# Kernel tuning notes

Hardware: AMD Instinct MI355X
Metric: run time of the kernel (lower is better)

Reference implementation:

```python
import jax, jax.numpy as jnp
import numpy as np
from jax import lax

K = 3        # kernel_size
PAD = 1      # padding
STRIDE = 1   # stride


def conv2d(x, w, stride, pad):
    return lax.conv_general_dilated(
        x, w, (stride, stride), [(pad, pad), (pad, pad)],
        dimension_numbers=('NCHW', 'OIHW', 'NCHW'))


def setup_inputs() -> dict:
    key = jax.random.key(0)
    ks = jax.random.split(key, 8)
    B, Ci, Cc, H, W = 8, 64, 64, 128, 128
    K2 = K * K
    return {
        'x_img': jax.random.normal(ks[0], (B, Ci, H, W), jnp.float32),
        'x_cont': jax.random.normal(ks[1], (B, Cc, H, W), jnp.float32),
        'w_fuse': jax.random.normal(ks[2], (Ci, Ci + Cc, 1, 1), jnp.float32) * 0.05,
        'w_off': jax.random.normal(ks[3], (2 * K2, Ci, K, K), jnp.float32) * 0.01,
        'b_off': jax.random.normal(ks[4], (2 * K2,), jnp.float32) * 0.1,
        'w_mod': jax.random.normal(ks[5], (K2, Ci, K, K), jnp.float32) * 0.01,
        'b_mod': jax.random.normal(ks[6], (K2,), jnp.float32) * 0.1,
        'w_reg': jax.random.normal(ks[7], (Ci, Ci, K, K), jnp.float32) * 0.05,
    }


def _bilinear_sample(img, py, px):
    # Zero padding outside the image (per-corner validity, matches torchvision).
    C, Hin, Win = img.shape
    flat = img.reshape(C, -1)
    y0 = jnp.floor(py)
    x0 = jnp.floor(px)

    def gather(yy, xx):
        valid = (yy >= 0) & (yy <= Hin - 1) & (xx >= 0) & (xx <= Win - 1)
        yc = jnp.clip(yy, 0, Hin - 1).astype(jnp.int32)
        xc = jnp.clip(xx, 0, Win - 1).astype(jnp.int32)
        return flat[:, yc * Win + xc] * valid[None].astype(img.dtype)

    wy1 = py - y0; wy0 = 1.0 - wy1
    wx1 = px - x0; wx0 = 1.0 - wx1
    return (gather(y0, x0) * (wy0 * wx0)[None]
            + gather(y0, x0 + 1.0) * (wy0 * wx1)[None]
            + gather(y0 + 1.0, x0) * (wy1 * wx0)[None]
            + gather(y0 + 1.0, x0 + 1.0) * (wy1 * wx1)[None])


def reference(x_img, x_cont, w_fuse, w_off, b_off, w_mod, b_mod, w_reg):
    # 1x1 fuse of image features with control factor
    x = conv2d(jnp.concatenate([x_img, x_cont], axis=1), w_fuse, 1, 0)
    # offset / modulator branches
    off = conv2d(x, w_off, STRIDE, PAD) + b_off[None, :, None, None]
    mod = 2.0 * jax.nn.sigmoid(conv2d(x, w_mod, STRIDE, PAD) + b_mod[None, :, None, None])
    B, C, Hin, Win = x.shape
    K2 = K * K
    Hout, Wout = off.shape[2], off.shape[3]
    # torchvision layout: channel 2k = dy, 2k+1 = dx for kernel pos k = i*K + j
    off = off.reshape(B, K2, 2, Hout, Wout)
    dy, dx = off[:, :, 0], off[:, :, 1]
    ky = (jnp.arange(K2) // K).astype(x.dtype)
    kx = (jnp.arange(K2) % K).astype(x.dtype)
    base_y = (jnp.arange(Hout) * STRIDE - PAD).astype(x.dtype)
    base_x = (jnp.arange(Wout) * STRIDE - PAD).astype(x.dtype)
    py = dy + base_y[None, None, :, None] + ky[None, :, None, None]  # [B,K2,H,W]
    px = dx + base_x[None, None, None, :] + kx[None, :, None, None]
    sampled = jax.vmap(_bilinear_sample)(x, py, px)          # [B,C,K2,H,W]
    sampled = sampled * mod[:, None]                          # modulation
    out = jnp.einsum('oik,bikhw->bohw', w_reg.reshape(C, C, K2), sampled)
    return out
```

## Files before the change

### kernel.cpp

```cpp
#include <hip/hip_runtime.h>
#include <math.h>

#define B_   8
#define C_   64
#define H_   128
#define W_   128
#define HW_  16384
#define K2_  9

typedef float f32x4 __attribute__((ext_vector_type(4)));
typedef short bf16x8 __attribute__((ext_vector_type(8)));
typedef unsigned short u16x4 __attribute__((ext_vector_type(4)));

#define WS_WFA  0
#define WS_WRP  8192
#define WS_WRP2 26624
#define WS_XT   45056
#define WS_OM   8433664

static __device__ __forceinline__ unsigned short f2bf(float x) {
    unsigned int u = __float_as_uint(x);
    unsigned int r = (u + 0x7fffu + ((u >> 16) & 1u)) >> 16;
    return (unsigned short)r;
}
static __device__ __forceinline__ float bf2f(unsigned short u) {
    return __uint_as_float(((unsigned int)u) << 16);
}

__global__ __launch_bounds__(256) void k_pack(const float* __restrict__ wf,
                                              const float* __restrict__ wreg,
                                              const float* __restrict__ wOff,
                                              const float* __restrict__ wMod,
                                              unsigned short* __restrict__ wfA,
                                              unsigned short* __restrict__ wrP,
                                              unsigned short* __restrict__ wrP2) {
    int idx = blockIdx.x * 256 + threadIdx.x;
    if (idx < 1024) {
        int lane = idx & 63, mt = (idx >> 6) & 3, kc = idx >> 8;
        int m = mt * 16 + (lane & 15);
        int kb = kc * 32 + (lane >> 4) * 8;
#pragma unroll
        for (int j = 0; j < 8; ++j)
            wfA[idx * 8 + j] = f2bf(wf[m * 128 + kb + j]);
    }
    if (idx < 4608) {
        int lane = idx & 63, mt = (idx >> 6) & 3, kc = (idx >> 8) & 1, tap = idx >> 9;
        int o = mt * 16 + (lane & 15);
        int ibase = kc * 32 + (lane >> 4) * 8;
#pragma unroll
        for (int j = 0; j < 8; ++j)
            wrP[idx * 8 + j] = f2bf(wreg[(o * 64 + ibase + j) * 9 + tap]);
    }
    if (idx < 2304) {
        int lane = idx & 63, mt = (idx >> 6) & 1, kc = idx >> 7;
        int m = mt * 16 + (lane & 15);
        int gkb = kc * 32 + (lane >> 4) * 8;
#pragma unroll
        for (int j = 0; j < 8; ++j) {
            int gk = gkb + j, tap = gk >> 6, ci = gk & 63;
            float v = 0.f;
            if (m < 18)      v = wOff[(m * 64 + ci) * 9 + tap];
            else if (m < 27) v = wMod[((m - 18) * 64 + ci) * 9 + tap];
            wrP2[idx * 8 + j] = f2bf(v);
        }
    }
}

__global__ __launch_bounds__(256) void k_fuse(const float* __restrict__ xi,
                                              const float* __restrict__ xc,
                                              const unsigned short* __restrict__ wfA,
                                              unsigned short* __restrict__ xtb) {
    const int t = threadIdx.x;
    const int lane = t & 63;
    const int wv = t >> 6;
    const int b = blockIdx.x & 7;
    const int yh = blockIdx.x >> 3;
    const int y = yh >> 1;
    const int h = yh & 1;

    const int n15 = lane & 15;
    const int q4 = lane >> 4;
    const int px = h * 64 + wv * 16 + n15;
    const size_t poff = (size_t)y * W_ + px;

    f32x4 acc[4];
#pragma unroll
    for (int mt = 0; mt < 4; ++mt) acc[mt] = (f32x4){0.f, 0.f, 0.f, 0.f};

#pragma unroll
    for (int kc = 0; kc < 4; ++kc) {
        const float* src = (kc < 2)
            ? (xi + ((size_t)(b * 64 + kc * 32 + q4 * 8)) * HW_ + poff)
            : (xc + ((size_t)(b * 64 + (kc - 2) * 32 + q4 * 8)) * HW_ + poff);
        unsigned short us[8];
#pragma unroll
        for (int j = 0; j < 8; ++j) us[j] = f2bf(src[(size_t)j * HW_]);
        const bf16x8 bf = *(const bf16x8*)us;
#pragma unroll
        for (int mt = 0; mt < 4; ++mt) {
            const bf16x8 a = *(const bf16x8*)(wfA + ((size_t)(kc * 4 + mt) * 64 + lane) * 8);
            acc[mt] = __builtin_amdgcn_mfma_f32_16x16x32_bf16(a, bf, acc[mt], 0, 0, 0);
        }
    }

#pragma unroll
    for (int mt = 0; mt < 4; ++mt) {
        u16x4 o4;
        o4.x = f2bf(acc[mt][0]); o4.y = f2bf(acc[mt][1]);
        o4.z = f2bf(acc[mt][2]); o4.w = f2bf(acc[mt][3]);
        *(u16x4*)&xtb[((size_t)b * HW_ + poff) * 64 + mt * 16 + q4 * 4] = o4;
    }
}

__global__ __launch_bounds__(256) void k_offmod(const unsigned short* __restrict__ xtb,
                                                const unsigned short* __restrict__ wrP2,
                                                const float* __restrict__ bOff,
                                                const float* __restrict__ bMod,
                                                float* __restrict__ om) {
    __shared__ unsigned short sB[3 * 66 * 72];
    const int t = threadIdx.x;
    const int lane = t & 63;
    const int wv = t >> 6;
    const int b = blockIdx.x & 7;
    const int yh = blockIdx.x >> 3;
    const int y = yh >> 1;
    const int h = yh & 1;

    for (int idx = t; idx < 3 * 66 * 8; idx += 256) {
        const int c8 = idx & 7;
        const int pp = (idx >> 3) % 66;
        const int row = (idx >> 3) / 66;
        const int gx = h * 64 + pp - 1;
        const int gy = y + row - 1;
        bf16x8 v = {0, 0, 0, 0, 0, 0, 0, 0};
        if (gx >= 0 && gx < W_ && gy >= 0 && gy < H_)
            v = *(const bf16x8*)&xtb[(((size_t)(b * H_ + gy)) * W_ + gx) * 64 + c8 * 8];
        *(bf16x8*)&sB[(row * 66 + pp) * 72 + c8 * 8] = v;
    }
    __syncthreads();

    const int n15 = lane & 15;
    const int q4 = lane >> 4;

    f32x4 acc[2];
    acc[0] = (f32x4){0.f, 0.f, 0.f, 0.f};
    acc[1] = (f32x4){0.f, 0.f, 0.f, 0.f};

#pragma unroll
    for (int kc = 0; kc < 18; ++kc) {
        const int gkb = kc * 32 + q4 * 8;
        const int tap = gkb >> 6;
        const int ci = gkb & 63;
        const int row = tap / 3, kx = tap % 3;
        const bf16x8 bf = *(const bf16x8*)&sB[(row * 66 + (wv * 16 + n15 + kx)) * 72 + ci];
        const bf16x8 a0 = *(const bf16x8*)(wrP2 + (((size_t)(kc * 2 + 0) * 64 + lane) * 8));
        const bf16x8 a1 = *(const bf16x8*)(wrP2 + (((size_t)(kc * 2 + 1) * 64 + lane) * 8));
        acc[0] = __builtin_amdgcn_mfma_f32_16x16x32_bf16(a0, bf, acc[0], 0, 0, 0);
        acc[1] = __builtin_amdgcn_mfma_f32_16x16x32_bf16(a1, bf, acc[1], 0, 0, 0);
    }

    const int px = h * 64 + wv * 16 + n15;
    const size_t rec = ((size_t)(b * H_ + y)) * 28 * 128;
#pragma unroll
    for (int mt = 0; mt < 2; ++mt)
#pragma unroll
        for (int r = 0; r < 4; ++r) {
            const int o = mt * 16 + q4 * 4 + r;
            if (o < 18) {
                const int c = (o >> 1) + ((o & 1) ? 9 : 0);
                om[rec + c * 128 + px] = acc[mt][r] + bOff[o];
            } else if (o < 27) {
                const float z = acc[mt][r] + bMod[o - 18];
                om[rec + (18 + (o - 18)) * 128 + px] = 2.f / (1.f + expf(-z));
            }
        }
}

__global__ __launch_bounds__(256) void k_deform(const unsigned short* __restrict__ xtb,
                                                const float* __restrict__ om,
                                                const unsigned short* __restrict__ wrP,
                                                float* __restrict__ out) {
    __shared__ unsigned short sS2[8 * 520];
    __shared__ unsigned int sRec[4 * 16 * 8];
    const int t = threadIdx.x;
    const int lane = t & 63;
    const int wv = t >> 6;
    const int b = blockIdx.x & 7;
    const int yh = blockIdx.x >> 3;
    const int y = yh >> 1;
    const int h = yh & 1;

    const char* xbB = (const char*)(xtb + (size_t)b * HW_ * 64);
    const float* omr = om + ((size_t)(b * H_ + y)) * 28 * 128;

    const int n15 = lane & 15;
    const int q4 = lane >> 4;
    const int pA = lane >> 2;
    const int corner = lane & 3;
    const int cy = corner >> 1, cx = corner & 1;

    f32x4 acc[4];
#pragma unroll
    for (int mt = 0; mt < 4; ++mt) acc[mt] = (f32x4){0.f, 0.f, 0.f, 0.f};

    for (int k = 0; k < 9; ++k) {
        const int ky = k / 3 - 1, kx = k % 3 - 1;

        {
            const int px = h * 64 + wv * 16 + pA;
            const float dy = omr[k * 128 + px];
            const float dxv = omr[(9 + k) * 128 + px];
            const float m = omr[(18 + k) * 128 + px];
            const float py  = (float)(y + ky) + dy;
            const float pxe = (float)(px + kx) + dxv;
            const float y0f = floorf(py), x0f = floorf(pxe);
            const int y0i = (int)y0f, x0i = (int)x0f;
            const float wy1 = py - y0f, wx1 = pxe - x0f;
            const int yy = y0i + cy;
            const int xx = x0i + cx;
            const bool ok = (yy >= 0) && (yy < H_) && (xx >= 0) && (xx < W_);
            const int yc = min(max(yy, 0), H_ - 1);
            const int xc = min(max(xx, 0), W_ - 1);
            const float w = (cy ? wy1 : 1.f - wy1) * (cx ? wx1 : 1.f - wx1) * m;
            uint2 rec;
            rec.x = (unsigned int)((yc * W_ + xc) * 128);
            rec.y = __float_as_uint(ok ? w : 0.f);
            *(uint2*)&sRec[((wv * 16 + pA) * 4 + corner) * 2] = rec;
        }

#pragma unroll 4
        for (int p = 0; p < 16; ++p) {
            const uint4 r0 = *(const uint4*)&sRec[(wv * 16 + p) * 8];
            const uint4 r1 = *(const uint4*)&sRec[(wv * 16 + p) * 8 + 4];
            const float g0 = bf2f(*(const unsigned short*)(xbB + (r0.x + lane * 2)));
            const float g1 = bf2f(*(const unsigned short*)(xbB + (r0.z + lane * 2)));
            const float g2 = bf2f(*(const unsigned short*)(xbB + (r1.x + lane * 2)));
            const float g3 = bf2f(*(const unsigned short*)(xbB + (r1.z + lane * 2)));
            const float v = g0 * __uint_as_float(r0.y) + g1 * __uint_as_float(r0.w)
                          + g2 * __uint_as_float(r1.y) + g3 * __uint_as_float(r1.w);
            sS2[(lane >> 3) * 520 + (wv * 16 + p) * 8 + (lane & 7)] = f2bf(v);
        }

#pragma unroll
        for (int kc = 0; kc < 2; ++kc) {
            const bf16x8 bf = *(const bf16x8*)&sS2[(kc * 4 + q4) * 520 + (wv * 16 + n15) * 8];
#pragma unroll
            for (int mt = 0; mt < 4; ++mt) {
                const bf16x8 a = *(const bf16x8*)(wrP +
                    ((((size_t)((k * 2 + kc) * 4 + mt)) * 64 + lane) * 8));
                acc[mt] = __builtin_amdgcn_mfma_f32_16x16x32_bf16(a, bf, acc[mt], 0, 0, 0);
            }
        }
    }

    const int px = h * 64 + wv * 16 + n15;
#pragma unroll
    for (int mt = 0; mt < 4; ++mt)
#pragma unroll
        for (int r = 0; r < 4; ++r) {
            const int o = mt * 16 + q4 * 4 + r;
            out[(((size_t)(b * 64 + o)) * H_ + y) * W_ + px] = acc[mt][r];
        }
}

extern "C" void kernel_launch(void* const* d_in, const int* in_sizes, int n_in,
                              void* d_out, int out_size, void* d_ws, size_t ws_size,
                              hipStream_t stream) {
    const float* x_img  = (const float*)d_in[0];
    const float* x_cont = (const float*)d_in[1];
    const float* w_fuse = (const float*)d_in[2];
    const float* w_off  = (const float*)d_in[3];
    const float* b_off  = (const float*)d_in[4];
    const float* w_mod  = (const float*)d_in[5];
    const float* b_mod  = (const float*)d_in[6];
    const float* w_reg  = (const float*)d_in[7];
    float* out = (float*)d_out;

    float* ws  = (float*)d_ws;
    unsigned short* wfA  = (unsigned short*)(ws + WS_WFA);
    unsigned short* wrP  = (unsigned short*)(ws + WS_WRP);
    unsigned short* wrP2 = (unsigned short*)(ws + WS_WRP2);
    unsigned short* xtb  = (unsigned short*)(ws + WS_XT);
    float* om  = ws + WS_OM;

    k_pack<<<18, 256, 0, stream>>>(w_fuse, w_reg, w_off, w_mod, wfA, wrP, wrP2);
    k_fuse<<<B_ * H_ * 2, 256, 0, stream>>>(x_img, x_cont, wfA, xtb);
    k_offmod<<<B_ * H_ * 2, 256, 0, stream>>>(xtb, wrP2, b_off, b_mod, om);
    k_deform<<<B_ * H_ * 2, 256, 0, stream>>>(xtb, om, wrP, out);
}
```

Before: 226.9 us.

## Fold weight packing into fuse kernel and use readlane for deform sample records

Removes the separate pack launch. The first 18 blocks of the fuse kernel now pack the regular and offset/modulator weights, and every block converts the 1x1 fuse weights into shared memory itself. The deform gather loop drops its shared-memory record buffer and broadcasts per-corner offsets and weights with readlane, and it is fully unrolled. The sigmoid uses the fast __expf. In exchange, every fuse block redoes the fuse-weight conversion, and the readlane-based scalar addressing depends on the compiler producing good code.

```diff
diff --git a/kernel.cpp b/kernel.cpp
--- a/kernel.cpp
+++ b/kernel.cpp
@@ -12,7 +12,6 @@
 typedef short bf16x8 __attribute__((ext_vector_type(8)));
 typedef unsigned short u16x4 __attribute__((ext_vector_type(4)));
 
-#define WS_WFA  0
 #define WS_WRP  8192
 #define WS_WRP2 26624
 #define WS_XT   45056
@@ -27,49 +26,16 @@
     return __uint_as_float(((unsigned int)u) << 16);
 }
 
-__global__ __launch_bounds__(256) void k_pack(const float* __restrict__ wf,
+__global__ __launch_bounds__(256) void k_fuse(const float* __restrict__ xi,
+                                              const float* __restrict__ xc,
+                                              const float* __restrict__ wf,
                                               const float* __restrict__ wreg,
                                               const float* __restrict__ wOff,
                                               const float* __restrict__ wMod,
-                                              unsigned short* __restrict__ wfA,
+                                              unsigned short* __restrict__ xtb,
                                               unsigned short* __restrict__ wrP,
                                               unsigned short* __restrict__ wrP2) {
-    int idx = blockIdx.x * 256 + threadIdx.x;
-    if (idx < 1024) {
-        int lane = idx & 63, mt = (idx >> 6) & 3, kc = idx >> 8;
-        int m = mt * 16 + (lane & 15);
-        int kb = kc * 32 + (lane >> 4) * 8;
-#pragma unroll
-        for (int j = 0; j < 8; ++j)
-            wfA[idx * 8 + j] = f2bf(wf[m * 128 + kb + j]);
-    }
-    if (idx < 4608) {
-        int lane = idx & 63, mt = (idx >> 6) & 3, kc = (idx >> 8) & 1, tap = idx >> 9;
-        int o = mt * 16 + (lane & 15);
-        int ibase = kc * 32 + (lane >> 4) * 8;
-#pragma unroll
-        for (int j = 0; j < 8; ++j)
-            wrP[idx * 8 + j] = f2bf(wreg[(o * 64 + ibase + j) * 9 + tap]);
-    }
-    if (idx < 2304) {
-        int lane = idx & 63, mt = (idx >> 6) & 1, kc = idx >> 7;
-        int m = mt * 16 + (lane & 15);
-        int gkb = kc * 32 + (lane >> 4) * 8;
-#pragma unroll
-        for (int j = 0; j < 8; ++j) {
-            int gk = gkb + j, tap = gk >> 6, ci = gk & 63;
-            float v = 0.f;
-            if (m < 18)      v = wOff[(m * 64 + ci) * 9 + tap];
-            else if (m < 27) v = wMod[((m - 18) * 64 + ci) * 9 + tap];
-            wrP2[idx * 8 + j] = f2bf(v);
-        }
-    }
-}
-
-__global__ __launch_bounds__(256) void k_fuse(const float* __restrict__ xi,
-                                              const float* __restrict__ xc,
-                                              const unsigned short* __restrict__ wfA,
-                                              unsigned short* __restrict__ xtb) {
+    __shared__ unsigned short sA[1024 * 8];
     const int t = threadIdx.x;
     const int lane = t & 63;
     const int wv = t >> 6;
@@ -78,6 +44,47 @@
     const int y = yh >> 1;
     const int h = yh & 1;
 
+    if (blockIdx.x < 18) {
+        const int idx = blockIdx.x * 256 + t;
+        if (idx < 4608) {
+            int ln = idx & 63, mt = (idx >> 6) & 3, kc = (idx >> 8) & 1, tap = idx >> 9;
+            int o = mt * 16 + (ln & 15);
+            int ibase = kc * 32 + (ln >> 4) * 8;
+#pragma unroll
+            for (int j = 0; j < 8; ++j)
+                wrP[idx * 8 + j] = f2bf(wreg[(o * 64 + ibase + j) * 9 + tap]);
+        }
+        if (idx < 2304) {
+            int ln = idx & 63, mt = (idx >> 6) & 1, kc = idx >> 7;
+            int m = mt * 16 + (ln & 15);
+            int gkb = kc * 32 + (ln >> 4) * 8;
+#pragma unroll
+            for (int j = 0; j < 8; ++j) {
+                int gk = gkb + j, tap = gk >> 6, ci = gk & 63;
+                float v = 0.f;
+                if (m < 18)      v = wOff[(m * 64 + ci) * 9 + tap];
+                else if (m < 27) v = wMod[((m - 18) * 64 + ci) * 9 + tap];
+                wrP2[idx * 8 + j] = f2bf(v);
+            }
+        }
+    }
+
+#pragma unroll
+    for (int r = 0; r < 4; ++r) {
+        const int c = t + 256 * r;
+        const int f = c >> 6;
+        const int ln = c & 63;
+        const int mt = f & 3, kc = f >> 2;
+        const int m = mt * 16 + (ln & 15);
+        const int kb = kc * 32 + (ln >> 4) * 8;
+        const float* s = wf + m * 128 + kb;
+        unsigned short us[8];
+#pragma unroll
+        for (int j = 0; j < 8; ++j) us[j] = f2bf(s[j]);
+        *(bf16x8*)&sA[c * 8] = *(const bf16x8*)us;
+    }
+    __syncthreads();
+
     const int n15 = lane & 15;
     const int q4 = lane >> 4;
     const int px = h * 64 + wv * 16 + n15;
@@ -98,7 +105,7 @@
         const bf16x8 bf = *(const bf16x8*)us;
 #pragma unroll
         for (int mt = 0; mt < 4; ++mt) {
-            const bf16x8 a = *(const bf16x8*)(wfA + ((size_t)(kc * 4 + mt) * 64 + lane) * 8);
+            const bf16x8 a = *(const bf16x8*)&sA[((kc * 4 + mt) * 64 + lane) * 8];
             acc[mt] = __builtin_amdgcn_mfma_f32_16x16x32_bf16(a, bf, acc[mt], 0, 0, 0);
         }
     }
@@ -171,7 +178,7 @@
                 om[rec + c * 128 + px] = acc[mt][r] + bOff[o];
             } else if (o < 27) {
                 const float z = acc[mt][r] + bMod[o - 18];
-                om[rec + (18 + (o - 18)) * 128 + px] = 2.f / (1.f + expf(-z));
+                om[rec + (18 + (o - 18)) * 128 + px] = 2.f / (1.f + __expf(-z));
             }
         }
 }
@@ -181,7 +188,6 @@
                                                 const unsigned short* __restrict__ wrP,
                                                 float* __restrict__ out) {
     __shared__ unsigned short sS2[8 * 520];
-    __shared__ unsigned int sRec[4 * 16 * 8];
     const int t = threadIdx.x;
     const int lane = t & 63;
     const int wv = t >> 6;
@@ -198,6 +204,8 @@
     const int pA = lane >> 2;
     const int corner = lane & 3;
     const int cy = corner >> 1, cx = corner & 1;
+    const int pxA = h * 64 + wv * 16 + pA;
+    const int gwrite = (lane >> 3) * 520 + (lane & 7);
 
     f32x4 acc[4];
 #pragma unroll
@@ -206,13 +214,14 @@
     for (int k = 0; k < 9; ++k) {
         const int ky = k / 3 - 1, kx = k % 3 - 1;
 
+        int rOff;
+        int rW;
         {
-            const int px = h * 64 + wv * 16 + pA;
-            const float dy = omr[k * 128 + px];
-            const float dxv = omr[(9 + k) * 128 + px];
-            const float m = omr[(18 + k) * 128 + px];
+            const float dy = omr[k * 128 + pxA];
+            const float dxv = omr[(9 + k) * 128 + pxA];
+            const float m = omr[(18 + k) * 128 + pxA];
             const float py  = (float)(y + ky) + dy;
-            const float pxe = (float)(px + kx) + dxv;
+            const float pxe = (float)(pxA + kx) + dxv;
             const float y0f = floorf(py), x0f = floorf(pxe);
             const int y0i = (int)y0f, x0i = (int)x0f;
             const float wy1 = py - y0f, wx1 = pxe - x0f;
@@ -222,23 +231,28 @@
             const int yc = min(max(yy, 0), H_ - 1);
             const int xc = min(max(xx, 0), W_ - 1);
             const float w = (cy ? wy1 : 1.f - wy1) * (cx ? wx1 : 1.f - wx1) * m;
-            uint2 rec;
-            rec.x = (unsigned int)((yc * W_ + xc) * 128);
-            rec.y = __float_as_uint(ok ? w : 0.f);
-            *(uint2*)&sRec[((wv * 16 + pA) * 4 + corner) * 2] = rec;
-        }
-
-#pragma unroll 4
+            rOff = (yc * W_ + xc) * 128;
+            rW = (int)__float_as_uint(ok ? w : 0.f);
+        }
+
+#pragma unroll
         for (int p = 0; p < 16; ++p) {
-            const uint4 r0 = *(const uint4*)&sRec[(wv * 16 + p) * 8];
-            const uint4 r1 = *(const uint4*)&sRec[(wv * 16 + p) * 8 + 4];
-            const float g0 = bf2f(*(const unsigned short*)(xbB + (r0.x + lane * 2)));
-            const float g1 = bf2f(*(const unsigned short*)(xbB + (r0.z + lane * 2)));
-            const float g2 = bf2f(*(const unsigned short*)(xbB + (r1.x + lane * 2)));
-            const float g3 = bf2f(*(const unsigned short*)(xbB + (r1.z + lane * 2)));
-            const float v = g0 * __uint_as_float(r0.y) + g1 * __uint_as_float(r0.w)
-                          + g2 * __uint_as_float(r1.y) + g3 * __uint_as_float(r1.w);
-            sS2[(lane >> 3) * 520 + (wv * 16 + p) * 8 + (lane & 7)] = f2bf(v);
+            const int l0 = p * 4;
+            const unsigned o0 = (unsigned)__builtin_amdgcn_readlane(rOff, l0 + 0);
+            const unsigned o1 = (unsigned)__builtin_amdgcn_readlane(rOff, l0 + 1);
+            const unsigned o2 = (unsigned)__builtin_amdgcn_readlane(rOff, l0 + 2);
+            const unsigned o3 = (unsigned)__builtin_amdgcn_readlane(rOff, l0 + 3);
+            const float w0 = __uint_as_float((unsigned)__builtin_amdgcn_readlane(rW, l0 + 0));
+            const float w1 = __uint_as_float((unsigned)__builtin_amdgcn_readlane(rW, l0 + 1));
+            const float w2 = __uint_as_float((unsigned)__builtin_amdgcn_readlane(rW, l0 + 2));
+            const float w3 = __uint_as_float((unsigned)__builtin_amdgcn_readlane(rW, l0 + 3));
+            const unsigned short* b0 = (const unsigned short*)(xbB + o0);
+            const unsigned short* b1 = (const unsigned short*)(xbB + o1);
+            const unsigned short* b2 = (const unsigned short*)(xbB + o2);
+            const unsigned short* b3 = (const unsigned short*)(xbB + o3);
+            const float v = bf2f(b0[lane]) * w0 + bf2f(b1[lane]) * w1
+                          + bf2f(b2[lane]) * w2 + bf2f(b3[lane]) * w3;
+            sS2[gwrite + (wv * 16 + p) * 8] = f2bf(v);
         }
 
 #pragma unroll
@@ -277,14 +291,13 @@
     float* out = (float*)d_out;
 
     float* ws  = (float*)d_ws;
-    unsigned short* wfA  = (unsigned short*)(ws + WS_WFA);
     unsigned short* wrP  = (unsigned short*)(ws + WS_WRP);
     unsigned short* wrP2 = (unsigned short*)(ws + WS_WRP2);
     unsigned short* xtb  = (unsigned short*)(ws + WS_XT);
     float* om  = ws + WS_OM;
 
-    k_pack<<<18, 256, 0, stream>>>(w_fuse, w_reg, w_off, w_mod, wfA, wrP, wrP2);
-    k_fuse<<<B_ * H_ * 2, 256, 0, stream>>>(x_img, x_cont, wfA, xtb);
+    k_fuse<<<B_ * H_ * 2, 256, 0, stream>>>(x_img, x_cont, w_fuse, w_reg, w_off,
+                                            w_mod, xtb, wrP, wrP2);
     k_offmod<<<B_ * H_ * 2, 256, 0, stream>>>(xtb, wrP2, b_off, b_mod, om);
     k_deform<<<B_ * H_ * 2, 256, 0, stream>>>(xtb, om, wrP, out);
 }
```

Result: faster. 216.5 us (-4.6%).
